# Performance work log

Measured on AMD Instinct MI355X. Metric: run time of the kernel, lower is better.

Reference implementation:

```python
import jax, jax.numpy as jnp
import numpy as np
import math
from functools import partial

SIGMA0 = 12.0
KSIZE = int(2 * (4.0 * SIGMA0 + 0.5))  # 97, already odd
if KSIZE % 2 == 0:
    KSIZE -= 1


def _gauss1d(ksize, sigma):
    # kornia-style gaussian; ksize is odd so no half-pixel shift
    x = jnp.arange(ksize, dtype=jnp.float32) - ksize // 2
    g = jnp.exp(-(x ** 2) / (2.0 * sigma ** 2))
    return g / g.sum()


def _blur(x, sigma):
    # x: (N,1,H,W). filter2d with outer(kx,ky) kernel and constant(zero) border
    # == two separable 1D convs with zero 'SAME' padding.
    k = _gauss1d(KSIZE, sigma)
    dn = ('NCHW', 'OIHW', 'NCHW')
    x = jax.lax.conv_general_dilated(x, k[None, None, :, None], (1, 1), 'SAME', dimension_numbers=dn)
    x = jax.lax.conv_general_dilated(x, k[None, None, None, :], (1, 1), 'SAME', dimension_numbers=dn)
    return x


def _grid_sample_bilinear(img, grid):
    # img: (N,C,H,W); grid: (N,H,W,2) with last dim (x,y) in [-1,1], align_corners=True
    N, C, H, W = img.shape
    x = (grid[..., 0] + 1.0) * 0.5 * (W - 1)
    y = (grid[..., 1] + 1.0) * 0.5 * (H - 1)
    x0 = jnp.floor(x); y0 = jnp.floor(y)
    wx = x - x0; wy = y - y0
    x0i = jnp.clip(x0, 0, W - 1).astype(jnp.int32)
    x1i = jnp.clip(x0 + 1, 0, W - 1).astype(jnp.int32)
    y0i = jnp.clip(y0, 0, H - 1).astype(jnp.int32)
    y1i = jnp.clip(y0 + 1, 0, H - 1).astype(jnp.int32)
    flat = img.reshape(N, C, H * W)

    def gather(yi, xi):
        idx = (yi * W + xi).reshape(N, 1, H * W)
        return jnp.take_along_axis(flat, idx, axis=2).reshape(N, C, H, W)

    wx = wx[:, None]; wy = wy[:, None]  # broadcast over C
    top = gather(y0i, x0i) * (1 - wx) + gather(y0i, x1i) * wx
    bot = gather(y1i, x0i) * (1 - wx) + gather(y1i, x1i) * wx
    return top * (1 - wy) + bot * wy


def _elastic(t, d_rand, sigma, alpha):
    # t: (1,C,H,W); d_rand: (1,2,H,W) uniform [0,1]
    n, c, h, w = t.shape
    d = d_rand * 2.0 - 1.0
    dy = _blur(d[:, 0:1], sigma[0]) * alpha[0]   # (1,1,H,W)
    dx = _blur(d[:, 1:2], sigma[1]) * alpha[1]
    d_yx = jnp.concatenate([dy, dx], axis=1).transpose(0, 2, 3, 1)  # (1,H,W,2) = (dy,dx)
    xs = jnp.linspace(-1.0, 1.0, w, dtype=t.dtype)
    ys = jnp.linspace(-1.0, 1.0, h, dtype=t.dtype)
    gx, gy = jnp.meshgrid(xs, ys)  # (H,W)
    grid = jnp.stack([gx, gy], axis=-1)[None]  # (1,H,W,2) (x,y)
    # NOTE: faithful to source: dy is added to x-coord, dx to y-coord
    return _grid_sample_bilinear(t, jnp.clip(grid + d_yx, -1.0, 1.0))


def setup_inputs() -> dict:
    key = jax.random.key(0)
    k1, k2, k3 = jax.random.split(key, 3)
    H = W = 2048
    return {
        'image': jax.random.normal(k1, (3, H, W), dtype=jnp.float32),
        'mask': (jax.random.uniform(k2, (1, H, W)) > 0.5).astype(jnp.float32),
        'd_rand': jax.random.uniform(k3, (1, 2, H, W), dtype=jnp.float32),
        'log_sigma': jnp.full((2,), math.log(12.0), dtype=jnp.float32),
        'log_alpha': jnp.zeros((2,), dtype=jnp.float32),
    }


def reference(image, mask, d_rand, log_sigma, log_alpha):
    sigma = jnp.exp(log_sigma)
    alpha = jnp.exp(log_alpha)
    img_out = _elastic(image[None], d_rand, sigma, alpha)[0]
    msk_out = _elastic(mask[None], d_rand, sigma, alpha)[0]
    return (img_out, msk_out)
```

## Files before the change

### kernel.cpp

```cpp
#include <hip/hip_runtime.h>

#define H 2048
#define W 2048
#define KS 97
#define KH 48
#define KPAD 112
#define TR 16
#define NB_VB 1024
#define NB_PK 4096

typedef float  nfloat4 __attribute__((ext_vector_type(4)));
typedef _Float16 h4v   __attribute__((ext_vector_type(4)));
typedef _Float16 h8v   __attribute__((ext_vector_type(8)));

__global__ __launch_bounds__(128) void make_weights_k(const float* __restrict__ log_sigma,
                                                      const float* __restrict__ log_alpha,
                                                      float* __restrict__ wts) {
    __shared__ float e0s[KS], e1s[KS];
    __shared__ float sums[2];
    const int t = threadIdx.x;
    const float s0 = expf(log_sigma[0]);
    const float s1 = expf(log_sigma[1]);
    if (t < KS) {
        const float xx = (float)(t - KH);
        e0s[t] = expf(-(xx * xx) / (2.f * s0 * s0));
        e1s[t] = expf(-(xx * xx) / (2.f * s1 * s1));
    }
    __syncthreads();
    if (t == 0) {
        float a = 0.f, b = 0.f;
        for (int k = 0; k < KS; ++k) { a += e0s[k]; b += e1s[k]; }
        sums[0] = a; sums[1] = b;
    }
    __syncthreads();
    if (t < KPAD) {
        wts[t]        = (t < KS) ? e0s[t] / sums[0] : 0.f;
        wts[KPAD + t] = (t < KS) ? e1s[t] / sums[1] : 0.f;
    }
    if (t == 0) {
        wts[2 * KPAD]     = expf(log_alpha[0]);
        wts[2 * KPAD + 1] = expf(log_alpha[1]);
    }
}

template <bool GUARD>
__device__ __forceinline__ float2 vload_row(const float* __restrict__ src, int row, int col) {
    float2 v = make_float2(0.f, 0.f);
    if (!GUARD || ((unsigned)row < (unsigned)H)) {
        const float2 r2 = *(const float2*)(src + (size_t)row * W + col);
        v.x = fmaf(r2.x, 2.f, -1.f);
        v.y = fmaf(r2.y, 2.f, -1.f);
    }
    return v;
}

template <bool GUARD>
__device__ __forceinline__ void vblur_body(const float* __restrict__ src,
                                           const float* __restrict__ g,
                                           float* __restrict__ dst,
                                           int col, int i0) {
    const int base = i0 - KH;
    float2 win[16];
    float2 acc[TR];
#pragma unroll
    for (int t = 0; t < TR; ++t) acc[t] = make_float2(0.f, 0.f);
#pragma unroll
    for (int t = 0; t < 15; ++t) win[t] = vload_row<GUARD>(src, base + t, col);

    for (int m = 0; m < KPAD / 16; ++m) {
        const int kb = m * 16;
#pragma unroll
        for (int r = 0; r < 16; ++r) {
            const int k = kb + r;
            win[(r + 15) & 15] = vload_row<GUARD>(src, base + k + 15, col);
            const float gk = g[k];
#pragma unroll
            for (int t = 0; t < TR; ++t) {
                const float2 u = win[(r + t) & 15];
                acc[t].x = fmaf(gk, u.x, acc[t].x);
                acc[t].y = fmaf(gk, u.y, acc[t].y);
            }
        }
    }
#pragma unroll
    for (int t = 0; t < TR; ++t)
        *(float2*)(dst + (size_t)(i0 + t) * W + col) = acc[t];
}

__global__ __launch_bounds__(256, 4) void pv_k(const float* __restrict__ drand,
                                               const float* __restrict__ wts,
                                               const float* __restrict__ image,
                                               const float* __restrict__ mask,
                                               float* __restrict__ tmp,
                                               h4v* __restrict__ packed) {
    const size_t HW = (size_t)H * W;
    const int bid = blockIdx.x;
    if (bid < NB_VB) {
        const int c   = bid >> 9;
        const int id  = bid & 511;
        const int xcd = id & 7;
        const int seq = id >> 3;
        const int yb  = xcd * 16 + (seq >> 2);
        const int xb  = seq & 3;
        const int col = (xb * 256 + threadIdx.x) * 2;
        const int i0  = yb * TR;
        const float* __restrict__ src = drand + (size_t)c * HW;
        const float* __restrict__ g   = wts + c * KPAD;
        float* __restrict__ dst       = tmp + (size_t)c * HW;
        if (i0 >= KH && i0 + 78 <= H - 1)
            vblur_body<false>(src, g, dst, col, i0);
        else
            vblur_body<true>(src, g, dst, col, i0);
    } else {
        const size_t idx4 = ((size_t)(bid - NB_VB) * 256 + threadIdx.x) * 4;
        const float4 p0 = *(const float4*)(image + idx4);
        const float4 p1 = *(const float4*)(image + HW + idx4);
        const float4 p2 = *(const float4*)(image + 2 * HW + idx4);
        const float4 pm = *(const float4*)(mask + idx4);
        h8v lo, hi;
        lo[0] = (_Float16)p0.x; lo[1] = (_Float16)p1.x; lo[2] = (_Float16)p2.x; lo[3] = (_Float16)pm.x;
        lo[4] = (_Float16)p0.y; lo[5] = (_Float16)p1.y; lo[6] = (_Float16)p2.y; lo[7] = (_Float16)pm.y;
        hi[0] = (_Float16)p0.z; hi[1] = (_Float16)p1.z; hi[2] = (_Float16)p2.z; hi[3] = (_Float16)pm.z;
        hi[4] = (_Float16)p0.w; hi[5] = (_Float16)p1.w; hi[6] = (_Float16)p2.w; hi[7] = (_Float16)pm.w;
        *(h8v*)(packed + idx4)     = lo;
        *(h8v*)(packed + idx4 + 2) = hi;
    }
}

#define SW 2160
template <bool PACKED>
__global__ __launch_bounds__(512) void hblur_sample_k(const float* __restrict__ tmp,
                                                      const float* __restrict__ wts,
                                                      const float* __restrict__ image,
                                                      const float* __restrict__ mask,
                                                      const h4v* __restrict__ packed,
                                                      float* __restrict__ out) {
    const int i   = (blockIdx.x & 7) * 256 + (blockIdx.x >> 3);
    const int tid = threadIdx.x;

    __shared__ __align__(16) float s0[SW];
    __shared__ __align__(16) float s1[SW];
    __shared__ __align__(16) float g0s[KPAD];
    __shared__ __align__(16) float g1s[KPAD];

    if (tid < KPAD) { g0s[tid] = wts[tid]; g1s[tid] = wts[KPAD + tid]; }

    const float* __restrict__ t0 = tmp + (size_t)i * W;
    const float* __restrict__ t1 = tmp + (size_t)H * W + (size_t)i * W;
    for (int idx = tid; idx < SW / 4; idx += 512) {
        const int colb = idx * 4 - KH;
        float4 v0 = make_float4(0.f, 0.f, 0.f, 0.f);
        float4 v1 = v0;
        if (colb >= 0 && colb + 3 < W) {
            v0 = *(const float4*)(t0 + colb);
            v1 = *(const float4*)(t1 + colb);
        }
        *(float4*)(s0 + idx * 4) = v0;
        *(float4*)(s1 + idx * 4) = v1;
    }
    __syncthreads();

    const int lb = tid * 4;

    float4 A0 = *(const float4*)(s0 + lb), B0 = *(const float4*)(s0 + lb + 4);
    float4 A1 = *(const float4*)(s1 + lb), B1 = *(const float4*)(s1 + lb + 4);
    float dy[4] = {0.f, 0.f, 0.f, 0.f}, dx[4] = {0.f, 0.f, 0.f, 0.f};

#pragma unroll
    for (int kg = 0; kg < 26; ++kg) {
        const int k0 = kg * 4;
        const float4 g0q = *(const float4*)(g0s + k0);
        const float4 g1q = *(const float4*)(g1s + k0);
        const float4 N0  = *(const float4*)(s0 + lb + k0 + 8);
        const float4 N1  = *(const float4*)(s1 + lb + k0 + 8);
        const float e0[8] = {A0.x, A0.y, A0.z, A0.w, B0.x, B0.y, B0.z, B0.w};
        const float e1[8] = {A1.x, A1.y, A1.z, A1.w, B1.x, B1.y, B1.z, B1.w};
#pragma unroll
        for (int j = 0; j < 4; ++j) {
            const float gj0 = j == 0 ? g0q.x : j == 1 ? g0q.y : j == 2 ? g0q.z : g0q.w;
            const float gj1 = j == 0 ? g1q.x : j == 1 ? g1q.y : j == 2 ? g1q.z : g1q.w;
#pragma unroll
            for (int c = 0; c < 4; ++c) {
                dy[c] = fmaf(gj0, e0[c + j], dy[c]);
                dx[c] = fmaf(gj1, e1[c + j], dx[c]);
            }
        }
        A0 = B0; B0 = N0; A1 = B1; B1 = N1;
    }

    const float a0 = wts[2 * KPAD];
    const float a1 = wts[2 * KPAD + 1];
    const float step = 2.f / 2047.f;
    float res[4][4];
#pragma unroll
    for (int c = 0; c < 4; ++c) {
        const int j = lb + c;
        const float dyc = dy[c] * a0;
        const float dxc = dx[c] * a1;
        float xn = -1.f + (float)j * step + dyc;
        float yn = -1.f + (float)i * step + dxc;
        xn = fminf(fmaxf(xn, -1.f), 1.f);
        yn = fminf(fmaxf(yn, -1.f), 1.f);

        const float x = (xn + 1.f) * 0.5f * (float)(W - 1);
        const float y = (yn + 1.f) * 0.5f * (float)(H - 1);
        const float x0f = floorf(x), y0f = floorf(y);
        const float wx = x - x0f, wy = y - y0f;

        int x0 = (int)x0f, y0 = (int)y0f;
        int x1 = x0 + 1, y1 = y0 + 1;
        x0 = min(max(x0, 0), W - 1); x1 = min(max(x1, 0), W - 1);
        y0 = min(max(y0, 0), H - 1); y1 = min(max(y1, 0), H - 1);

        const float w00 = (1.f - wx) * (1.f - wy);
        const float w10 = wx * (1.f - wy);
        const float w01 = (1.f - wx) * wy;
        const float w11 = wx * wy;

        const size_t i00 = (size_t)y0 * W + x0;
        const size_t i10 = (size_t)y0 * W + x1;
        const size_t i01 = (size_t)y1 * W + x0;
        const size_t i11 = (size_t)y1 * W + x1;

        if (PACKED) {
            const h4v v00 = packed[i00], v10 = packed[i10];
            const h4v v01 = packed[i01], v11 = packed[i11];
            res[0][c] = (float)v00[0] * w00 + (float)v10[0] * w10 + (float)v01[0] * w01 + (float)v11[0] * w11;
            res[1][c] = (float)v00[1] * w00 + (float)v10[1] * w10 + (float)v01[1] * w01 + (float)v11[1] * w11;
            res[2][c] = (float)v00[2] * w00 + (float)v10[2] * w10 + (float)v01[2] * w01 + (float)v11[2] * w11;
            res[3][c] = (float)v00[3] * w00 + (float)v10[3] * w10 + (float)v01[3] * w01 + (float)v11[3] * w11;
        } else {
#pragma unroll
            for (int p = 0; p < 3; ++p) {
                const float* __restrict__ pl = image + (size_t)p * H * W;
                res[p][c] = pl[i00] * w00 + pl[i10] * w10 + pl[i01] * w01 + pl[i11] * w11;
            }
            res[3][c] = mask[i00] * w00 + mask[i10] * w10 + mask[i01] * w01 + mask[i11] * w11;
        }
    }

    const size_t o = (size_t)i * W + lb;
#pragma unroll
    for (int p = 0; p < 4; ++p) {
        nfloat4 v;
        v.x = res[p][0]; v.y = res[p][1]; v.z = res[p][2]; v.w = res[p][3];
        __builtin_nontemporal_store(v, (nfloat4*)(out + (size_t)p * H * W + o));
    }
}

extern "C" void kernel_launch(void* const* d_in, const int* in_sizes, int n_in,
                              void* d_out, int out_size, void* d_ws, size_t ws_size,
                              hipStream_t stream) {
    const float* image     = (const float*)d_in[0];
    const float* mask      = (const float*)d_in[1];
    const float* drand     = (const float*)d_in[2];
    const float* log_sigma = (const float*)d_in[3];
    const float* log_alpha = (const float*)d_in[4];
    float* out = (float*)d_out;

    const size_t HW = (size_t)H * W;
    const bool can_pack = ws_size >= HW * 8 + 2 * HW * 4 + 1024;

    h4v* packed; float* tmp; float* wts;
    if (can_pack) {
        packed = (h4v*)d_ws;
        tmp    = (float*)((char*)d_ws + HW * 8);
        wts    = tmp + 2 * HW;
    } else {
        packed = nullptr;
        tmp    = (float*)d_ws;
        wts    = tmp + 2 * HW;
    }

    make_weights_k<<<1, 128, 0, stream>>>(log_sigma, log_alpha, wts);
    pv_k<<<can_pack ? (NB_VB + NB_PK) : NB_VB, 256, 0, stream>>>(drand, wts, image, mask,
                                                                 tmp, packed);
    if (can_pack)
        hblur_sample_k<true><<<H, 512, 0, stream>>>(tmp, wts, image, mask, packed, out);
    else
        hblur_sample_k<false><<<H, 512, 0, stream>>>(tmp, wts, image, mask, packed, out);
}
```

Measured before the change: 236.0 us.

## Restructure vertical blur into fully unrolled 8-row groups with prefetch ring

Replaces the 16-entry rolling window and runtime loop over K in the vertical blur with four rotating 8-row register buffers. The 97-tap loop is now fully unrolled, and the next group of rows is loaded one group ahead of the FMAs that consume it. This removes dynamic index arithmetic, skips loads beyond the 97 real taps, and lets the fast unguarded path cover more row blocks. Launch bounds are relaxed from 4 to 3 blocks per SM to give the compiler more registers, at the cost of occupancy.

New measurement: 244.6 us. +3.7%, slower.

```diff
diff --git a/kernel.cpp b/kernel.cpp
--- a/kernel.cpp
+++ b/kernel.cpp
@@ -54,32 +54,66 @@
     return v;
 }
 
+template <bool GUARD, int M>
+__device__ __forceinline__ void vgroup8(const float* __restrict__ src, int col, int base,
+                                        const float* __restrict__ g,
+                                        float2 (&c0)[8], float2 (&c1)[8], float2 (&c2)[8],
+                                        float2 (&fut)[8], float2 (&acc)[TR]) {
+#pragma unroll
+    for (int j = 0; j < 8; ++j) {
+        if (8 * M + 24 + j <= 111)
+            fut[j] = vload_row<GUARD>(src, base + 8 * M + 24 + j, col);
+    }
+#pragma unroll
+    for (int r = 0; r < 8; ++r) {
+        const float gk = g[8 * M + r];
+#pragma unroll
+        for (int t = 0; t < TR; ++t) {
+            const int w = r + t;
+            const float2 u = (w < 8) ? c0[w] : (w < 16) ? c1[w - 8] : c2[w - 16];
+            acc[t].x = fmaf(gk, u.x, acc[t].x);
+            acc[t].y = fmaf(gk, u.y, acc[t].y);
+        }
+    }
+}
+
 template <bool GUARD>
 __device__ __forceinline__ void vblur_body(const float* __restrict__ src,
                                            const float* __restrict__ g,
                                            float* __restrict__ dst,
                                            int col, int i0) {
     const int base = i0 - KH;
-    float2 win[16];
+    float2 D0[8], D1[8], D2[8], D3[8];
     float2 acc[TR];
 #pragma unroll
     for (int t = 0; t < TR; ++t) acc[t] = make_float2(0.f, 0.f);
 #pragma unroll
-    for (int t = 0; t < 15; ++t) win[t] = vload_row<GUARD>(src, base + t, col);
-
-    for (int m = 0; m < KPAD / 16; ++m) {
-        const int kb = m * 16;
-#pragma unroll
-        for (int r = 0; r < 16; ++r) {
-            const int k = kb + r;
-            win[(r + 15) & 15] = vload_row<GUARD>(src, base + k + 15, col);
-            const float gk = g[k];
-#pragma unroll
-            for (int t = 0; t < TR; ++t) {
-                const float2 u = win[(r + t) & 15];
-                acc[t].x = fmaf(gk, u.x, acc[t].x);
-                acc[t].y = fmaf(gk, u.y, acc[t].y);
-            }
+    for (int j = 0; j < 8; ++j) D0[j] = vload_row<GUARD>(src, base + j, col);
+#pragma unroll
+    for (int j = 0; j < 8; ++j) D1[j] = vload_row<GUARD>(src, base + 8 + j, col);
+#pragma unroll
+    for (int j = 0; j < 8; ++j) D2[j] = vload_row<GUARD>(src, base + 16 + j, col);
+
+    vgroup8<GUARD, 0>(src, col, base, g, D0, D1, D2, D3, acc);
+    vgroup8<GUARD, 1>(src, col, base, g, D1, D2, D3, D0, acc);
+    vgroup8<GUARD, 2>(src, col, base, g, D2, D3, D0, D1, acc);
+    vgroup8<GUARD, 3>(src, col, base, g, D3, D0, D1, D2, acc);
+    vgroup8<GUARD, 4>(src, col, base, g, D0, D1, D2, D3, acc);
+    vgroup8<GUARD, 5>(src, col, base, g, D1, D2, D3, D0, acc);
+    vgroup8<GUARD, 6>(src, col, base, g, D2, D3, D0, D1, acc);
+    vgroup8<GUARD, 7>(src, col, base, g, D3, D0, D1, D2, acc);
+    vgroup8<GUARD, 8>(src, col, base, g, D0, D1, D2, D3, acc);
+    vgroup8<GUARD, 9>(src, col, base, g, D1, D2, D3, D0, acc);
+    vgroup8<GUARD, 10>(src, col, base, g, D2, D3, D0, D1, acc);
+    vgroup8<GUARD, 11>(src, col, base, g, D3, D0, D1, D2, acc);
+
+    {
+        const float gk = g[96];
+#pragma unroll
+        for (int t = 0; t < TR; ++t) {
+            const float2 u = (t < 8) ? D0[t] : D1[t - 8];
+            acc[t].x = fmaf(gk, u.x, acc[t].x);
+            acc[t].y = fmaf(gk, u.y, acc[t].y);
         }
     }
 #pragma unroll
@@ -87,7 +121,7 @@
         *(float2*)(dst + (size_t)(i0 + t) * W + col) = acc[t];
 }
 
-__global__ __launch_bounds__(256, 4) void pv_k(const float* __restrict__ drand,
+__global__ __launch_bounds__(256, 3) void pv_k(const float* __restrict__ drand,
                                                const float* __restrict__ wts,
                                                const float* __restrict__ image,
                                                const float* __restrict__ mask,
@@ -107,7 +141,7 @@
         const float* __restrict__ src = drand + (size_t)c * HW;
         const float* __restrict__ g   = wts + c * KPAD;
         float* __restrict__ dst       = tmp + (size_t)c * HW;
-        if (i0 >= KH && i0 + 78 <= H - 1)
+        if (i0 >= KH && i0 + 63 <= H - 1)
             vblur_body<false>(src, g, dst, col, i0);
         else
             vblur_body<true>(src, g, dst, col, i0);
```

## Fold the 2x-1 affine map out of the blur and shrink the kernel tail

Applied to the files above, without the earlier changes.

The per-sample 2*d-1 transform is moved out of the vertical blur loads. Zero padding becomes padding with 0.5, and the affine map is applied once after both blurs as 2*alpha*sum - alpha, which is valid because the weights are normalized. The vertical blur now uses a 24-entry register ring and runs only the 97 real taps instead of 112 padded ones, with a tighter condition for the unguarded path. This removes per-load FMAs and wasted zero-weight taps, at the cost of more registers and a result that depends on the weights summing exactly to one.

Measured after the change: 229.7 us. 1.03x faster.

```diff
diff --git a/kernel.cpp b/kernel.cpp
--- a/kernel.cpp
+++ b/kernel.cpp
@@ -6,6 +6,7 @@
 #define KH 48
 #define KPAD 112
 #define TR 16
+#define RING 24
 #define NB_VB 1024
 #define NB_PK 4096
 
@@ -45,12 +46,11 @@
 
 template <bool GUARD>
 __device__ __forceinline__ float2 vload_row(const float* __restrict__ src, int row, int col) {
-    float2 v = make_float2(0.f, 0.f);
-    if (!GUARD || ((unsigned)row < (unsigned)H)) {
-        const float2 r2 = *(const float2*)(src + (size_t)row * W + col);
-        v.x = fmaf(r2.x, 2.f, -1.f);
-        v.y = fmaf(r2.y, 2.f, -1.f);
-    }
+    if (!GUARD)
+        return *(const float2*)(src + (size_t)row * W + col);
+    float2 v = make_float2(0.5f, 0.5f);
+    if ((unsigned)row < (unsigned)H)
+        v = *(const float2*)(src + (size_t)row * W + col);
     return v;
 }
 
@@ -60,26 +60,47 @@
                                            float* __restrict__ dst,
                                            int col, int i0) {
     const int base = i0 - KH;
-    float2 win[16];
+    float2 win[RING];
     float2 acc[TR];
 #pragma unroll
     for (int t = 0; t < TR; ++t) acc[t] = make_float2(0.f, 0.f);
 #pragma unroll
-    for (int t = 0; t < 15; ++t) win[t] = vload_row<GUARD>(src, base + t, col);
-
-    for (int m = 0; m < KPAD / 16; ++m) {
-        const int kb = m * 16;
-#pragma unroll
-        for (int r = 0; r < 16; ++r) {
-            const int k = kb + r;
-            win[(r + 15) & 15] = vload_row<GUARD>(src, base + k + 15, col);
-            const float gk = g[k];
+    for (int j = 0; j < RING; ++j) win[j] = vload_row<GUARD>(src, base + j, col);
+
+    for (int m = 0; m < 3; ++m) {
+        const int kb = m * 24;
+#pragma unroll
+        for (int r = 0; r < 24; ++r) {
+            const float gk = g[kb + r];
 #pragma unroll
             for (int t = 0; t < TR; ++t) {
-                const float2 u = win[(r + t) & 15];
-                acc[t].x = fmaf(gk, u.x, acc[t].x);
-                acc[t].y = fmaf(gk, u.y, acc[t].y);
+                const int w = (r + t) < 24 ? (r + t) : (r + t - 24);
+                acc[t].x = fmaf(gk, win[w].x, acc[t].x);
+                acc[t].y = fmaf(gk, win[w].y, acc[t].y);
             }
+            win[r] = vload_row<GUARD>(src, base + kb + r + 24, col);
+        }
+    }
+    {
+#pragma unroll
+        for (int r = 0; r < 24; ++r) {
+            const float gk = g[72 + r];
+#pragma unroll
+            for (int t = 0; t < TR; ++t) {
+                const int w = (r + t) < 24 ? (r + t) : (r + t - 24);
+                acc[t].x = fmaf(gk, win[w].x, acc[t].x);
+                acc[t].y = fmaf(gk, win[w].y, acc[t].y);
+            }
+            if (r <= 15)
+                win[r] = vload_row<GUARD>(src, base + 96 + r, col);
+        }
+    }
+    {
+        const float gk = g[96];
+#pragma unroll
+        for (int t = 0; t < TR; ++t) {
+            acc[t].x = fmaf(gk, win[t].x, acc[t].x);
+            acc[t].y = fmaf(gk, win[t].y, acc[t].y);
         }
     }
 #pragma unroll
@@ -107,7 +128,7 @@
         const float* __restrict__ src = drand + (size_t)c * HW;
         const float* __restrict__ g   = wts + c * KPAD;
         float* __restrict__ dst       = tmp + (size_t)c * HW;
-        if (i0 >= KH && i0 + 78 <= H - 1)
+        if (i0 >= KH && i0 + 63 <= H - 1)
             vblur_body<false>(src, g, dst, col, i0);
         else
             vblur_body<true>(src, g, dst, col, i0);
@@ -149,7 +170,7 @@
     const float* __restrict__ t1 = tmp + (size_t)H * W + (size_t)i * W;
     for (int idx = tid; idx < SW / 4; idx += 512) {
         const int colb = idx * 4 - KH;
-        float4 v0 = make_float4(0.f, 0.f, 0.f, 0.f);
+        float4 v0 = make_float4(0.5f, 0.5f, 0.5f, 0.5f);
         float4 v1 = v0;
         if (colb >= 0 && colb + 3 < W) {
             v0 = *(const float4*)(t0 + colb);
@@ -190,13 +211,15 @@
 
     const float a0 = wts[2 * KPAD];
     const float a1 = wts[2 * KPAD + 1];
+    const float a0x2 = a0 + a0;
+    const float a1x2 = a1 + a1;
     const float step = 2.f / 2047.f;
     float res[4][4];
 #pragma unroll
     for (int c = 0; c < 4; ++c) {
         const int j = lb + c;
-        const float dyc = dy[c] * a0;
-        const float dxc = dx[c] * a1;
+        const float dyc = fmaf(dy[c], a0x2, -a0);
+        const float dxc = fmaf(dx[c], a1x2, -a1);
         float xn = -1.f + (float)j * step + dyc;
         float yn = -1.f + (float)i * step + dxc;
         xn = fminf(fmaxf(xn, -1.f), 1.f);
```
